# Kernel optimization log

Hardware: AMD Instinct MI355X
Metric: run time of the kernel (lower is better)

Reference implementation:

```python
import jax, jax.numpy as jnp
import numpy as np

DIM = 1024
NUM_HEADS = 16
HEAD_DIM = DIM // NUM_HEADS
SCALE = float(np.sqrt(HEAD_DIM))
NEG = -1e9


def setup_inputs() -> dict:
    key = jax.random.key(0)
    ks = jax.random.split(key, 12)
    B, S = 2, 2048
    std = 1.0 / np.sqrt(DIM)
    inp = {
        'query': jax.random.normal(ks[0], (B, S, DIM), jnp.float32),
        'key': jax.random.normal(ks[1], (B, S, DIM), jnp.float32),
        'value': jax.random.normal(ks[2], (B, S, DIM), jnp.float32),
        'key_padding_mask': jnp.ones((B, S), jnp.int32),
        'Wq': jax.random.normal(ks[3], (DIM, DIM), jnp.float32) * std,
        'bq': jax.random.normal(ks[4], (DIM,), jnp.float32) * std,
        'Wk': jax.random.normal(ks[5], (DIM, DIM), jnp.float32) * std,
        'bk': jax.random.normal(ks[6], (DIM,), jnp.float32) * std,
        'Wv': jax.random.normal(ks[7], (DIM, DIM), jnp.float32) * std,
        'bv': jax.random.normal(ks[8], (DIM,), jnp.float32) * std,
        'Wo': jax.random.normal(ks[9], (DIM, DIM), jnp.float32) * std,
        'bo': jax.random.normal(ks[10], (DIM,), jnp.float32) * std,
    }
    return inp


def reference(query, key, value, key_padding_mask, Wq, bq, Wk, bk, Wv, bv, Wo, bo):
    B, S, _ = query.shape
    # QKV projections (torch Linear: x @ W.T + b), split heads -> [B,H,S,D]
    def proj(x, W, b):
        return (x @ W.T + b).reshape(B, -1, NUM_HEADS, HEAD_DIM).transpose(0, 2, 1, 3)
    Q = proj(query, Wq, bq)
    K = proj(key, Wk, bk)
    V = proj(value, Wv, bv)
    # scaled dot-product scores [B,H,Sq,Sk]
    scores = jnp.einsum('bhqd,bhkd->bhqk', Q, K) / SCALE
    # key padding mask: positions where mask == 0 are filled with -1e9
    pad = (key_padding_mask == 0)[:, None, None, :]  # [B,1,1,Sk]
    scores = jnp.where(pad, NEG, scores)
    attention_weights = jax.nn.softmax(scores, axis=-1)
    context = jnp.einsum('bhqk,bhkd->bhqd', attention_weights, V)
    context = context.transpose(0, 2, 1, 3).reshape(B, -1, DIM)
    out = context @ Wo.T + bo
    return out, attention_weights
```

## Files before the change

kernel.cpp:

```cpp
#include <hip/hip_runtime.h>
#include <hip/hip_bf16.h>
#include <stdint.h>

#define DIMM 1024
#define HEADS 16
#define HD 64
#define BB 2
#define SS 2048
#define NTOK (BB*SS)

typedef __attribute__((ext_vector_type(8))) __bf16 bf16x8;
typedef __attribute__((ext_vector_type(4))) __bf16 bf16x4;
typedef __attribute__((ext_vector_type(4))) float f32x4;

__device__ __forceinline__ f32x4 mfma16(bf16x8 a, bf16x8 b, f32x4 c) {
  return __builtin_amdgcn_mfma_f32_16x16x32_bf16(a, b, c, 0, 0, 0);
}

__device__ __forceinline__ void gload_lds16(const void* g, void* l) {
  __builtin_amdgcn_global_load_lds(
      (__attribute__((address_space(1))) void*)(void*)g,
      (__attribute__((address_space(3))) void*)l,
      16, 0, 0);
}

#define LOG2E 1.4426950408889634f
#define C2 (0.125f * LOG2E)
#define NBRAW (-8e9f)

struct CvtArgs {
  const float* src[7];
  __bf16* dst[7];
  int n[7];
};

__global__ __launch_bounds__(256) void cvt_kernel(CvtArgs a) {
  const int t = blockIdx.y;
  const long i = ((long)blockIdx.x * 256 + threadIdx.x) * 8;
  if (i >= a.n[t]) return;
  const float* s = a.src[t] + i;
  f32x4 x0 = *(const f32x4*)s;
  f32x4 x1 = *(const f32x4*)(s + 4);
  bf16x8 o;
  o[0] = (__bf16)x0[0]; o[1] = (__bf16)x0[1]; o[2] = (__bf16)x0[2]; o[3] = (__bf16)x0[3];
  o[4] = (__bf16)x1[0]; o[5] = (__bf16)x1[1]; o[6] = (__bf16)x1[2]; o[7] = (__bf16)x1[3];
  *(bf16x8*)(a.dst[t] + i) = o;
}

__global__ void maskbits_kernel(const int* __restrict__ msk, uint32_t* __restrict__ mbits) {
  int j = threadIdx.x;
  if (j >= 128) return;
  const int* src = msk + j * 32;
  uint32_t wdd = 0;
#pragma unroll
  for (int i = 0; i < 32; ++i) wdd |= (src[i] != 0 ? 1u : 0u) << i;
  mbits[j] = wdd;
}

struct GemmArgs {
  const __bf16* A[3];
  const __bf16* B[3];
  const float* bias[3];
  void* out[3];
  int mode[3];
};

__global__ __launch_bounds__(256) void gemm_bt(GemmArgs ga) {
  const int z = blockIdx.z;
  const __bf16* __restrict__ A  = ga.A[z];
  const __bf16* __restrict__ Bm = ga.B[z];
  const float* __restrict__ bias = ga.bias[z];
  void* Cout = ga.out[z];
  const int mode = ga.mode[z];

  __shared__ __align__(16) char sA[2][16384];
  __shared__ __align__(16) char sB[2][16384];
  const int tid = threadIdx.x;
  const int w = tid >> 6, l = tid & 63;
  const int wr = w >> 1, wc = w & 1;
  const int lg = l >> 4, lr = l & 15;
  const int m0 = blockIdx.y * 128, n0 = blockIdx.x * 128;

  f32x4 acc[4][4] = {};

  auto stage = [&](int k0, int buf) {
#pragma unroll
    for (int i = 0; i < 4; ++i) {
      int c = (i * 4 + w) * 64 + l;
      int row = c >> 3, ch = c & 7;
      gload_lds16(A + (size_t)(m0 + row) * 1024 + k0 + ((ch ^ (row & 7)) << 3),
                  &sA[buf][(i * 4 + w) * 1024]);
    }
#pragma unroll
    for (int i = 0; i < 4; ++i) {
      int c = (i * 4 + w) * 64 + l;
      int row = c >> 3, ch = c & 7;
      gload_lds16(Bm + (size_t)(n0 + row) * 1024 + k0 + ((ch ^ (row & 7)) << 3),
                  &sB[buf][(i * 4 + w) * 1024]);
    }
  };

  stage(0, 0);
  __syncthreads();

  for (int ks = 0; ks < 16; ++ks) {
    const int cur = ks & 1;
    if (ks < 15) stage((ks + 1) * 64, cur ^ 1);
#pragma unroll
    for (int kk = 0; kk < 2; ++kk) {
      bf16x8 af[4], bfv[4];
#pragma unroll
      for (int fm = 0; fm < 4; ++fm) {
        int row = wr * 64 + fm * 16 + lr;
        af[fm] = *(const bf16x8*)&sA[cur][row * 128 + (((kk * 4 + lg) ^ (row & 7)) << 4)];
      }
#pragma unroll
      for (int fn = 0; fn < 4; ++fn) {
        int row = wc * 64 + fn * 16 + lr;
        bfv[fn] = *(const bf16x8*)&sB[cur][row * 128 + (((kk * 4 + lg) ^ (row & 7)) << 4)];
      }
#pragma unroll
      for (int fm = 0; fm < 4; ++fm)
#pragma unroll
        for (int fn = 0; fn < 4; ++fn)
          acc[fm][fn] = mfma16(af[fm], bfv[fn], acc[fm][fn]);
    }
    __syncthreads();
  }

#pragma unroll
  for (int fm = 0; fm < 4; ++fm) {
#pragma unroll
    for (int fn = 0; fn < 4; ++fn) {
      const int n = n0 + wc * 64 + fn * 16 + lr;
      const int mb = m0 + wr * 64 + fm * 16 + 4 * lg;
      const float bval = bias[n];
      f32x4 vv = acc[fm][fn];
      if (mode == 2) {
        float* C = (float*)Cout;
#pragma unroll
        for (int r = 0; r < 4; ++r)
          C[(size_t)(mb + r) * 1024 + n] = vv[r] + bval;
      } else if (mode == 0) {
        __bf16* C = (__bf16*)Cout;
        const int hh = n >> 6, d = n & 63;
#pragma unroll
        for (int r = 0; r < 4; ++r) {
          int m = mb + r;
          C[(((size_t)(m >> 11) * 16 + hh) * 2048 + (m & 2047)) * 64 + d] =
              (__bf16)(vv[r] + bval);
        }
      } else {
        __bf16* C = (__bf16*)Cout;
        const int hh = n >> 6, d = n & 63;
        bf16x4 pk;
#pragma unroll
        for (int r = 0; r < 4; ++r) pk[r] = (__bf16)(vv[r] + bval);
        *(bf16x4*)(C + (((size_t)(mb >> 11) * 16 + hh) * 64 + d) * 2048 + (mb & 2047)) = pk;
      }
    }
  }
}

__global__ __launch_bounds__(256) void attn_kernel(
    const __bf16* __restrict__ Qh, const __bf16* __restrict__ Kh,
    const __bf16* __restrict__ Vt, const uint32_t* __restrict__ mbits,
    float* __restrict__ attnW, __bf16* __restrict__ ctx)
{
  __shared__ __align__(16) char sK[2][8192];
  __shared__ __align__(16) char sV[2][8192];
  __shared__ __align__(16) float sPF[4][16][64];

  const int tid = threadIdx.x;
  const int w = tid >> 6, l = tid & 63;
  const int lg = l >> 4, lr = l & 15;

  const int bid = blockIdx.x;
  const int xcd = bid & 7, j = bid >> 3;
  const int bh = xcd * 4 + (j >> 5);
  const int q0 = (j & 31) * 64;
  const int b = bh >> 4, h = bh & 15;

  const __bf16* qbase = Qh + ((size_t)bh * SS + q0 + w * 16 + lr) * HD;
  bf16x8 qf0 = *(const bf16x8*)(qbase + lg * 8);
  bf16x8 qf1 = *(const bf16x8*)(qbase + 32 + lg * 8);

  const __bf16* Khead = Kh + (size_t)bh * SS * HD;
  const __bf16* Vhead = Vt + (size_t)bh * HD * SS;
  const uint32_t* mrow = mbits + b * 64;

  const int c0 = w * 64 + l;

  auto stageK = [&](int k0, int buf) {
#pragma unroll
    for (int i = 0; i < 2; ++i) {
      int c = i * 256 + c0;
      int kr = c >> 3, ch = c & 7;
      gload_lds16(Khead + (size_t)(k0 + kr) * HD + ((ch ^ (kr & 7)) << 3),
                  &sK[buf][(i * 4 + w) * 1024]);
    }
  };
  auto stageV = [&](int k0, int buf) {
#pragma unroll
    for (int i = 0; i < 2; ++i) {
      int c = i * 256 + c0;
      int d = c >> 3, ch = c & 7;
      gload_lds16(Vhead + (size_t)d * SS + k0 + ((ch ^ (d & 7)) << 3),
                  &sV[buf][(i * 4 + w) * 1024]);
    }
  };

  stageK(0, 0);
  asm volatile("s_waitcnt vmcnt(0)" ::: "memory");
  __builtin_amdgcn_s_barrier();

  float lsum = 0.0f;

  for (int t = 0; t < 32; ++t) {
    const int cur = t & 1;
    if (t < 31) stageK((t + 1) * 64, cur ^ 1);

    const uint32_t mw0 = mrow[2 * t], mw1 = mrow[2 * t + 1];
    const bool fast = ((mw0 & mw1) == 0xFFFFFFFFu);

#pragma unroll
    for (int sub = 0; sub < 4; ++sub) {
      const int kr = sub * 16 + lr;
      bf16x8 k0f = *(const bf16x8*)&sK[cur][kr * 128 + ((lg ^ (kr & 7)) << 4)];
      bf16x8 k1f = *(const bf16x8*)&sK[cur][kr * 128 + (((4 + lg) ^ (kr & 7)) << 4)];
      __builtin_amdgcn_s_setprio(1);
      f32x4 a = {};
      a = mfma16(k0f, qf0, a);
      a = mfma16(k1f, qf1, a);
      __builtin_amdgcn_s_setprio(0);
      if (!fast) {
        uint32_t bits = ((sub < 2) ? mw0 : mw1) >> ((sub & 1) * 16 + 4 * lg);
#pragma unroll
        for (int r = 0; r < 4; ++r) a[r] = ((bits >> r) & 1) ? a[r] : NBRAW;
      }
#pragma unroll
      for (int r = 0; r < 4; ++r)
        lsum += __builtin_amdgcn_exp2f(fminf(a[r] * C2, 80.0f));
    }
    asm volatile("s_waitcnt vmcnt(0)" ::: "memory");
    __builtin_amdgcn_s_barrier();
  }

  lsum += __shfl_xor(lsum, 16);
  lsum += __shfl_xor(lsum, 32);
  const float rl = 1.0f / lsum;

  f32x4 Oa[4] = {};
  float* pwbase = attnW + ((size_t)bh * SS + q0 + w * 16) * SS;

  stageK(0, 0);
  stageV(0, 0);
  asm volatile("s_waitcnt vmcnt(0)" ::: "memory");
  __builtin_amdgcn_s_barrier();

  for (int t = 0; t < 32; ++t) {
    const int cur = t & 1;
    if (t < 31) { stageK((t + 1) * 64, cur ^ 1); stageV((t + 1) * 64, cur ^ 1); }

    const uint32_t mw0 = mrow[2 * t], mw1 = mrow[2 * t + 1];
    const bool fast = ((mw0 & mw1) == 0xFFFFFFFFu);

#pragma unroll
    for (int sub = 0; sub < 4; ++sub) {
      const int kr = sub * 16 + lr;
      bf16x8 k0f = *(const bf16x8*)&sK[cur][kr * 128 + ((lg ^ (kr & 7)) << 4)];
      bf16x8 k1f = *(const bf16x8*)&sK[cur][kr * 128 + (((4 + lg) ^ (kr & 7)) << 4)];
      __builtin_amdgcn_s_setprio(1);
      f32x4 a = {};
      a = mfma16(k0f, qf0, a);
      a = mfma16(k1f, qf1, a);
      __builtin_amdgcn_s_setprio(0);
      if (!fast) {
        uint32_t bits = ((sub < 2) ? mw0 : mw1) >> ((sub & 1) * 16 + 4 * lg);
#pragma unroll
        for (int r = 0; r < 4; ++r) a[r] = ((bits >> r) & 1) ? a[r] : NBRAW;
      }
      f32x4 p;
#pragma unroll
      for (int r = 0; r < 4; ++r)
        p[r] = __builtin_amdgcn_exp2f(fminf(a[r] * C2, 80.0f)) * rl;
      const int cp = (sub * 4 + lg) ^ (lr & 7);
      *(f32x4*)&sPF[w][lr][cp * 4] = p;
    }

#pragma unroll
    for (int i = 0; i < 4; ++i) {
      const int row = i * 4 + lg;
      const int cp = lr ^ (row & 7);
      f32x4 pv4 = *(const f32x4*)&sPF[w][row][cp * 4];
      __builtin_nontemporal_store(pv4,
          (f32x4*)(pwbase + (size_t)row * SS + t * 64 + lr * 4));
    }

#pragma unroll
    for (int hh = 0; hh < 2; ++hh) {
      f32x4 pa_lo = *(const f32x4*)&sPF[w][lr][(((hh * 8 + 2 * lg) ^ (lr & 7)) * 4)];
      f32x4 pa_hi = *(const f32x4*)&sPF[w][lr][(((hh * 8 + 2 * lg + 1) ^ (lr & 7)) * 4)];
      bf16x8 pa;
#pragma unroll
      for (int r = 0; r < 4; ++r) {
        pa[r] = (__bf16)pa_lo[r];
        pa[4 + r] = (__bf16)pa_hi[r];
      }
      __builtin_amdgcn_s_setprio(1);
#pragma unroll
      for (int dg = 0; dg < 4; ++dg) {
        const int d = dg * 16 + lr;
        bf16x8 vb = *(const bf16x8*)&sV[cur][d * 128 + (((hh * 4 + lg) ^ (d & 7)) << 4)];
        Oa[dg] = mfma16(pa, vb, Oa[dg]);
      }
      __builtin_amdgcn_s_setprio(0);
    }

    asm volatile("s_waitcnt vmcnt(4)" ::: "memory");
    __builtin_amdgcn_s_barrier();
  }

#pragma unroll
  for (int dg = 0; dg < 4; ++dg)
#pragma unroll
    for (int r = 0; r < 4; ++r)
      ctx[(size_t)(b * SS + q0 + w * 16 + 4 * lg + r) * DIMM + h * HD + dg * 16 + lr] =
          (__bf16)Oa[dg][r];
}

extern "C" void kernel_launch(void* const* d_in, const int* in_sizes, int n_in,
                              void* d_out, int out_size, void* d_ws, size_t ws_size,
                              hipStream_t stream)
{
  const float* q   = (const float*)d_in[0];
  const float* k   = (const float*)d_in[1];
  const float* v   = (const float*)d_in[2];
  const int*   msk = (const int*)d_in[3];
  const float* Wq  = (const float*)d_in[4];
  const float* bq  = (const float*)d_in[5];
  const float* Wk  = (const float*)d_in[6];
  const float* bk  = (const float*)d_in[7];
  const float* Wv  = (const float*)d_in[8];
  const float* bv  = (const float*)d_in[9];
  const float* Wo  = (const float*)d_in[10];
  const float* bo  = (const float*)d_in[11];

  char* ws = (char*)d_ws;
  __bf16* xq  = (__bf16*)(ws);
  __bf16* xk  = (__bf16*)(ws + (8u << 20));
  __bf16* xv  = (__bf16*)(ws + (16u << 20));
  __bf16* wqb = (__bf16*)(ws + (24u << 20));
  __bf16* wkb = (__bf16*)(ws + (26u << 20));
  __bf16* wvb = (__bf16*)(ws + (28u << 20));
  __bf16* wob = (__bf16*)(ws + (30u << 20));
  __bf16* Qh  = (__bf16*)(ws + (32u << 20));
  __bf16* Kh  = (__bf16*)(ws + (40u << 20));
  __bf16* Vt  = (__bf16*)(ws + (48u << 20));
  __bf16* ctx = (__bf16*)(ws + (56u << 20));
  uint32_t* mbits = (uint32_t*)(ws + (64u << 20));

  CvtArgs ca;
  ca.src[0] = q;  ca.dst[0] = xq;  ca.n[0] = NTOK * DIMM;
  ca.src[1] = k;  ca.dst[1] = xk;  ca.n[1] = NTOK * DIMM;
  ca.src[2] = v;  ca.dst[2] = xv;  ca.n[2] = NTOK * DIMM;
  ca.src[3] = Wq; ca.dst[3] = wqb; ca.n[3] = DIMM * DIMM;
  ca.src[4] = Wk; ca.dst[4] = wkb; ca.n[4] = DIMM * DIMM;
  ca.src[5] = Wv; ca.dst[5] = wvb; ca.n[5] = DIMM * DIMM;
  ca.src[6] = Wo; ca.dst[6] = wob; ca.n[6] = DIMM * DIMM;
  cvt_kernel<<<dim3(2048, 7, 1), 256, 0, stream>>>(ca);
  maskbits_kernel<<<1, 128, 0, stream>>>(msk, mbits);

  GemmArgs g1;
  g1.A[0] = xq; g1.B[0] = wqb; g1.bias[0] = bq; g1.out[0] = (void*)Qh; g1.mode[0] = 0;
  g1.A[1] = xk; g1.B[1] = wkb; g1.bias[1] = bk; g1.out[1] = (void*)Kh; g1.mode[1] = 0;
  g1.A[2] = xv; g1.B[2] = wvb; g1.bias[2] = bv; g1.out[2] = (void*)Vt; g1.mode[2] = 1;
  gemm_bt<<<dim3(8, 32, 3), 256, 0, stream>>>(g1);

  float* out = (float*)d_out;
  float* attnW = out + (size_t)NTOK * DIMM;
  attn_kernel<<<dim3(1024, 1, 1), 256, 0, stream>>>(Qh, Kh, Vt, mbits, attnW, ctx);

  GemmArgs g2;
  g2.A[0] = ctx; g2.B[0] = wob; g2.bias[0] = bo; g2.out[0] = (void*)out; g2.mode[0] = 2;
  g2.A[1] = ctx; g2.B[1] = wob; g2.bias[1] = bo; g2.out[1] = (void*)out; g2.mode[1] = 2;
  g2.A[2] = ctx; g2.B[2] = wob; g2.bias[2] = bo; g2.out[2] = (void*)out; g2.mode[2] = 2;
  gemm_bt<<<dim3(8, 32, 1), 256, 0, stream>>>(g2);
}
```

Before: 269.8 us.

## Load K and V fragments directly from global memory instead of LDS staging

Removes the double-buffered async global-to-LDS staging of K and V tiles in the attention kernel, and with it the per-iteration waitcnt and workgroup barriers. Each wave now reads its MFMA operands for K and V straight from global memory, relying on L1/L2 caching since all four waves read the same tiles. This cuts LDS use and synchronisation, but each wave issues its own global loads. There is no longer any prefetch to hide their latency behind the MFMA and exp work.

```diff
diff --git a/kernel.cpp b/kernel.cpp
--- a/kernel.cpp
+++ b/kernel.cpp
@@ -167,8 +167,6 @@
     const __bf16* __restrict__ Vt, const uint32_t* __restrict__ mbits,
     float* __restrict__ attnW, __bf16* __restrict__ ctx)
 {
-  __shared__ __align__(16) char sK[2][8192];
-  __shared__ __align__(16) char sV[2][8192];
   __shared__ __align__(16) float sPF[4][16][64];
 
   const int tid = threadIdx.x;
@@ -189,45 +187,18 @@
   const __bf16* Vhead = Vt + (size_t)bh * HD * SS;
   const uint32_t* mrow = mbits + b * 64;
 
-  const int c0 = w * 64 + l;
-
-  auto stageK = [&](int k0, int buf) {
-#pragma unroll
-    for (int i = 0; i < 2; ++i) {
-      int c = i * 256 + c0;
-      int kr = c >> 3, ch = c & 7;
-      gload_lds16(Khead + (size_t)(k0 + kr) * HD + ((ch ^ (kr & 7)) << 3),
-                  &sK[buf][(i * 4 + w) * 1024]);
-    }
-  };
-  auto stageV = [&](int k0, int buf) {
-#pragma unroll
-    for (int i = 0; i < 2; ++i) {
-      int c = i * 256 + c0;
-      int d = c >> 3, ch = c & 7;
-      gload_lds16(Vhead + (size_t)d * SS + k0 + ((ch ^ (d & 7)) << 3),
-                  &sV[buf][(i * 4 + w) * 1024]);
-    }
-  };
-
-  stageK(0, 0);
-  asm volatile("s_waitcnt vmcnt(0)" ::: "memory");
-  __builtin_amdgcn_s_barrier();
-
   float lsum = 0.0f;
 
   for (int t = 0; t < 32; ++t) {
-    const int cur = t & 1;
-    if (t < 31) stageK((t + 1) * 64, cur ^ 1);
-
+    const int k0 = t * 64;
     const uint32_t mw0 = mrow[2 * t], mw1 = mrow[2 * t + 1];
     const bool fast = ((mw0 & mw1) == 0xFFFFFFFFu);
 
 #pragma unroll
     for (int sub = 0; sub < 4; ++sub) {
-      const int kr = sub * 16 + lr;
-      bf16x8 k0f = *(const bf16x8*)&sK[cur][kr * 128 + ((lg ^ (kr & 7)) << 4)];
-      bf16x8 k1f = *(const bf16x8*)&sK[cur][kr * 128 + (((4 + lg) ^ (kr & 7)) << 4)];
+      const __bf16* kp = Khead + (size_t)(k0 + sub * 16 + lr) * HD + lg * 8;
+      bf16x8 k0f = *(const bf16x8*)kp;
+      bf16x8 k1f = *(const bf16x8*)(kp + 32);
       __builtin_amdgcn_s_setprio(1);
       f32x4 a = {};
       a = mfma16(k0f, qf0, a);
@@ -242,8 +213,6 @@
       for (int r = 0; r < 4; ++r)
         lsum += __builtin_amdgcn_exp2f(fminf(a[r] * C2, 80.0f));
     }
-    asm volatile("s_waitcnt vmcnt(0)" ::: "memory");
-    __builtin_amdgcn_s_barrier();
   }
 
   lsum += __shfl_xor(lsum, 16);
@@ -253,23 +222,16 @@
   f32x4 Oa[4] = {};
   float* pwbase = attnW + ((size_t)bh * SS + q0 + w * 16) * SS;
 
-  stageK(0, 0);
-  stageV(0, 0);
-  asm volatile("s_waitcnt vmcnt(0)" ::: "memory");
-  __builtin_amdgcn_s_barrier();
-
   for (int t = 0; t < 32; ++t) {
-    const int cur = t & 1;
-    if (t < 31) { stageK((t + 1) * 64, cur ^ 1); stageV((t + 1) * 64, cur ^ 1); }
-
+    const int k0 = t * 64;
     const uint32_t mw0 = mrow[2 * t], mw1 = mrow[2 * t + 1];
     const bool fast = ((mw0 & mw1) == 0xFFFFFFFFu);
 
 #pragma unroll
     for (int sub = 0; sub < 4; ++sub) {
-      const int kr = sub * 16 + lr;
-      bf16x8 k0f = *(const bf16x8*)&sK[cur][kr * 128 + ((lg ^ (kr & 7)) << 4)];
-      bf16x8 k1f = *(const bf16x8*)&sK[cur][kr * 128 + (((4 + lg) ^ (kr & 7)) << 4)];
+      const __bf16* kp = Khead + (size_t)(k0 + sub * 16 + lr) * HD + lg * 8;
+      bf16x8 k0f = *(const bf16x8*)kp;
+      bf16x8 k1f = *(const bf16x8*)(kp + 32);
       __builtin_amdgcn_s_setprio(1);
       f32x4 a = {};
       a = mfma16(k0f, qf0, a);
@@ -294,7 +256,7 @@
       const int cp = lr ^ (row & 7);
       f32x4 pv4 = *(const f32x4*)&sPF[w][row][cp * 4];
       __builtin_nontemporal_store(pv4,
-          (f32x4*)(pwbase + (size_t)row * SS + t * 64 + lr * 4));
+          (f32x4*)(pwbase + (size_t)row * SS + k0 + lr * 4));
     }
 
 #pragma unroll
@@ -311,14 +273,11 @@
 #pragma unroll
       for (int dg = 0; dg < 4; ++dg) {
         const int d = dg * 16 + lr;
-        bf16x8 vb = *(const bf16x8*)&sV[cur][d * 128 + (((hh * 4 + lg) ^ (d & 7)) << 4)];
+        bf16x8 vb = *(const bf16x8*)(Vhead + (size_t)d * SS + k0 + (hh * 4 + lg) * 8);
         Oa[dg] = mfma16(pa, vb, Oa[dg]);
       }
       __builtin_amdgcn_s_setprio(0);
     }
-
-    asm volatile("s_waitcnt vmcnt(4)" ::: "memory");
-    __builtin_amdgcn_s_barrier();
   }
 
 #pragma unroll
```

After: 450.2 us. 1.67x slower.
